# Kernel optimization log

Hardware: AMD Instinct MI355X
Metric: run time of the kernel (lower is better)

The kernel has to match this reference:

```python
import jax, jax.numpy as jnp
import numpy as np

FIELD_DIMS = [100000, 1000, 100, 50]
NUM_FEATURES = 12
NUM_CAT = len(FIELD_DIMS)
NUM_CONT = NUM_FEATURES - NUM_CAT
D = 32            # embed_dim
HID = [64, 32]
B, T = 1024, 200
BN_EPS = 1e-5


def setup_inputs() -> dict:
    key = jax.random.key(0)
    ks = jax.random.split(key, 32)
    # x: [B, T, F]; first NUM_CAT cols are integer category ids stored as float
    cat_cols = [jax.random.randint(ks[i], (B, T, 1), 0, FIELD_DIMS[i]).astype(jnp.float32)
                for i in range(NUM_CAT)]
    cont_cols = jax.random.normal(ks[4], (B, T, NUM_CONT), dtype=jnp.float32)
    x = jnp.concatenate(cat_cols + [cont_cols], axis=-1)
    s = 0.05
    inp = {"x": x}
    for i, fd in enumerate(FIELD_DIMS):
        inp[f"emb{i}"] = jax.random.normal(ks[5 + i], (fd, D), dtype=jnp.float32) * s
        inp[f"lin{i}"] = jax.random.normal(ks[9 + i], (fd, D), dtype=jnp.float32) * s
    # Conv1d(1, D, 1) per continuous field == per-field affine map scalar -> D
    inp["cont_w"]  = jax.random.normal(ks[13], (NUM_CONT, D), dtype=jnp.float32) * s
    inp["cont_b"]  = jax.random.normal(ks[14], (NUM_CONT, D), dtype=jnp.float32) * s
    inp["clin_w"]  = jax.random.normal(ks[15], (NUM_CONT, D), dtype=jnp.float32) * s
    inp["clin_b"]  = jax.random.normal(ks[16], (NUM_CONT, D), dtype=jnp.float32) * s
    inp["fin_bias"] = jnp.zeros((D,), dtype=jnp.float32)
    # DNN tower: kernel_size-1 Conv1d == dense over channel dim
    dims = [NUM_FEATURES * D] + HID
    for li in range(len(HID)):
        fan_in = dims[li]
        inp[f"w{li+1}"] = jax.random.normal(ks[17 + 4 * li], (HID[li], fan_in), dtype=jnp.float32) / np.sqrt(fan_in)
        inp[f"b{li+1}"] = jnp.zeros((HID[li],), dtype=jnp.float32)
        inp[f"g{li+1}"] = jnp.ones((HID[li],), dtype=jnp.float32)
        inp[f"beta{li+1}"] = jnp.zeros((HID[li],), dtype=jnp.float32)
    inp["w_out"] = jax.random.normal(ks[30], (D, HID[-1]), dtype=jnp.float32) / np.sqrt(HID[-1])
    inp["b_out"] = jnp.zeros((D,), dtype=jnp.float32)
    return inp


def _batchnorm(h, g, b):
    # training-mode BN over (batch, time), biased variance (torch default)
    mu = h.mean(axis=(0, 1))
    var = h.var(axis=(0, 1))
    return g * (h - mu) * jax.lax.rsqrt(var + BN_EPS) + b


def reference(x, emb0, emb1, emb2, emb3, lin0, lin1, lin2, lin3,
              cont_w, cont_b, clin_w, clin_b, fin_bias,
              w1, b1, g1, beta1, w2, b2, g2, beta2, w_out, b_out):
    embs = [emb0, emb1, emb2, emb3]
    lins = [lin0, lin1, lin2, lin3]
    cat_idx = x[..., :NUM_CAT].astype(jnp.int32)          # [B,T,C]
    xc = x[..., NUM_CAT:]                                  # [B,T,Nc]

    # per-field embeddings -> [B,T,F,D]
    cat_emb = jnp.stack([embs[i][cat_idx[..., i]] for i in range(NUM_CAT)], axis=2)
    cont_emb = xc[..., None] * cont_w + cont_b             # [B,T,Nc,D]
    emb_all = jnp.concatenate([cat_emb, cont_emb], axis=2)  # [B,T,F,D]

    # FM pairwise interaction (sum-of-squares trick)
    s = emb_all.sum(axis=2)                                # [B,T,D]
    interaction = 0.5 * (s * s - (emb_all * emb_all).sum(axis=2))

    # linear terms
    lin_cat = sum(lins[i][cat_idx[..., i]] for i in range(NUM_CAT))      # [B,T,D]
    lin_cont = (xc[..., None] * clin_w + clin_b).sum(axis=2)             # [B,T,D]
    linear = lin_cat + lin_cont + fin_bias

    # DNN tower (k=1 convs == dense over F*D channels); dropout omitted (eval)
    h = emb_all.reshape(B, T, NUM_FEATURES * D)
    h = jax.nn.relu(_batchnorm(h @ w1.T + b1, g1, beta1))
    h = jax.nn.relu(_batchnorm(h @ w2.T + b2, g2, beta2))
    dnn = h @ w_out.T + b_out                              # [B,T,D]

    return linear + interaction + dnn                      # [B,T,D]
```

## Files before the change

kernel.cpp:

```cpp
#include <hip/hip_runtime.h>
#include <hip/hip_bf16.h>

typedef __hip_bfloat16 bf16;

#define ROWS 204800
#define N_INV (1.0f / 204800.0f)

__device__ float g_stats[256];
__device__ float g_E1_1[1000 * 64];
__device__ float g_E1_2[100 * 64];
__device__ float g_E1_3[50 * 64];
__device__ float g_U[8 * 64];
__device__ float g_Vb[64];
__device__ bf16  g_h1p[ROWS * 64];
__device__ bf16  g_h2p[ROWS * 32];

__device__ __forceinline__ int clampi(int v, int hi) {
    return v < 0 ? 0 : (v > hi ? hi : v);
}

__global__ __launch_bounds__(64) void precompute_kernel(
    const float* __restrict__ emb1, const float* __restrict__ emb2, const float* __restrict__ emb3,
    const float* __restrict__ cont_w, const float* __restrict__ cont_b,
    const float* __restrict__ w1, const float* __restrict__ b1)
{
    int b = blockIdx.x;
    int k = threadIdx.x;
    __shared__ float row[32];

    if (b < 1150) {
        const float* tab; float* out; int i, colOff;
        if (b < 1000)      { tab = emb1; out = g_E1_1; i = b;        colOff = 32; }
        else if (b < 1100) { tab = emb2; out = g_E1_2; i = b - 1000; colOff = 64; }
        else               { tab = emb3; out = g_E1_3; i = b - 1100; colOff = 96; }
        if (k < 32) row[k] = tab[i * 32 + k];
        __syncthreads();
        const float* wr = w1 + k * 384 + colOff;
        float acc = 0.f;
        #pragma unroll
        for (int d = 0; d < 32; ++d) acc = fmaf(row[d], wr[d], acc);
        out[i * 64 + k] = acc;
    } else {
        g_stats[k]       = 0.f;
        g_stats[k + 64]  = 0.f;
        g_stats[k + 128] = 0.f;
        g_stats[k + 192] = 0.f;

        float vb = b1[k];
        #pragma unroll
        for (int j = 0; j < 8; ++j) {
            const float* wr = w1 + k * 384 + (4 + j) * 32;
            float u = 0.f;
            #pragma unroll
            for (int d = 0; d < 32; ++d) {
                float w = wr[d];
                u  = fmaf(cont_w[j * 32 + d], w, u);
                vb = fmaf(cont_b[j * 32 + d], w, vb);
            }
            g_U[j * 64 + k] = u;
        }
        g_Vb[k] = vb;
    }
}

__global__ __launch_bounds__(256) void phase1_kernel(
    const float* __restrict__ x,
    const float* __restrict__ emb0, const float* __restrict__ lin0,
    const float* __restrict__ emb1, const float* __restrict__ lin1,
    const float* __restrict__ emb2, const float* __restrict__ lin2,
    const float* __restrict__ emb3, const float* __restrict__ lin3,
    const float* __restrict__ cont_w, const float* __restrict__ cont_b,
    const float* __restrict__ clin_w, const float* __restrict__ clin_b,
    const float* __restrict__ fin_bias, const float* __restrict__ w1,
    float* __restrict__ fm_out)
{
    __shared__ float lsum[64], lsq[64];

    int tid  = threadIdx.x;
    int lane = tid & 63;
    int wv   = tid >> 6;
    int d    = lane & 31;
    bool lo  = lane < 32;

    if (tid < 64) { lsum[tid] = 0.f; lsq[tid] = 0.f; }
    __syncthreads();

    float w1col[32];
    {
        const float4* wr = (const float4*)(w1 + lane * 384);
        #pragma unroll
        for (int q = 0; q < 8; ++q) {
            float4 v = wr[q];
            w1col[4*q+0] = v.x; w1col[4*q+1] = v.y;
            w1col[4*q+2] = v.z; w1col[4*q+3] = v.w;
        }
    }
    float uk[8];
    #pragma unroll
    for (int j = 0; j < 8; ++j) uk[j] = g_U[j * 64 + lane];
    float vbk = g_Vb[lane];

    float p1[8], p2[8], fb = 0.f;
    if (lo) {
        #pragma unroll
        for (int j = 0; j < 8; ++j) { p1[j] = cont_w[j * 32 + d]; p2[j] = cont_b[j * 32 + d]; }
    } else {
        #pragma unroll
        for (int j = 0; j < 8; ++j) { p1[j] = clin_w[j * 32 + d]; p2[j] = clin_b[j * 32 + d]; }
        fb = fin_bias[d];
    }

    int gw   = blockIdx.x * 4 + wv;
    int base = gw * 25;
    float ss = 0.f, qq = 0.f;

    float xv = (lane < 12) ? x[base * 12 + lane] : 0.f;

    for (int it = 0; it < 25; ++it) {
        int r = base + it;

        int i0 = clampi((int)__shfl(xv, 0), 99999);
        int i1 = clampi((int)__shfl(xv, 1), 999);
        int i2 = clampi((int)__shfl(xv, 2), 99);
        int i3 = clampi((int)__shfl(xv, 3), 49);
        float xc[8];
        #pragma unroll
        for (int j = 0; j < 8; ++j) xc[j] = __shfl(xv, 4 + j);

        float ga, gb, gc, gd;
        if (lo) {
            ga = emb0[i0 * 32 + d]; gb = emb1[i1 * 32 + d];
            gc = emb2[i2 * 32 + d]; gd = emb3[i3 * 32 + d];
        } else {
            ga = lin0[i0 * 32 + d]; gb = lin1[i1 * 32 + d];
            gc = lin2[i2 * 32 + d]; gd = lin3[i3 * 32 + d];
        }
        float t1 = g_E1_1[i1 * 64 + lane];
        float t2 = g_E1_2[i2 * 64 + lane];
        float t3 = g_E1_3[i3 * 64 + lane];
        float xvn = (it < 24 && lane < 12) ? x[(r + 1) * 12 + lane] : 0.f;

        float half_val;
        if (lo) {
            float s = (ga + gb) + (gc + gd);
            float q = fmaf(ga, ga, gb * gb) + fmaf(gc, gc, gd * gd);
            #pragma unroll
            for (int j = 0; j < 8; ++j) {
                float ce = fmaf(xc[j], p1[j], p2[j]);
                s += ce;
                q = fmaf(ce, ce, q);
            }
            half_val = 0.5f * (s * s - q);
        } else {
            float l = (ga + gb) + (gc + gd) + fb;
            #pragma unroll
            for (int j = 0; j < 8; ++j) l = fmaf(xc[j], p1[j], l + p2[j]);
            half_val = l;
        }
        float other = __shfl(half_val, lane | 32);
        if (lo) fm_out[r * 32 + d] = half_val + other;

        float h1 = ((vbk + t1) + (t2 + t3));
        #pragma unroll
        for (int j = 0; j < 8; ++j) h1 = fmaf(xc[j], uk[j], h1);

        float a0 = 0.f, a1 = 0.f, a2 = 0.f, a3 = 0.f;
        #pragma unroll
        for (int dd = 0; dd < 32; dd += 4) {
            a0 = fmaf(__shfl(ga, dd + 0), w1col[dd + 0], a0);
            a1 = fmaf(__shfl(ga, dd + 1), w1col[dd + 1], a1);
            a2 = fmaf(__shfl(ga, dd + 2), w1col[dd + 2], a2);
            a3 = fmaf(__shfl(ga, dd + 3), w1col[dd + 3], a3);
        }
        h1 += (a0 + a1) + (a2 + a3);

        g_h1p[r * 64 + lane] = __float2bfloat16(h1);
        ss += h1;
        qq = fmaf(h1, h1, qq);
        xv = xvn;
    }

    atomicAdd(&lsum[lane], ss);
    atomicAdd(&lsq[lane], qq);
    __syncthreads();
    if (tid < 64) {
        atomicAdd(&g_stats[tid], lsum[tid]);
        atomicAdd(&g_stats[64 + tid], lsq[tid]);
    }
}

__global__ __launch_bounds__(256) void phase2_kernel(
    const float* __restrict__ w2, const float* __restrict__ b2,
    const float* __restrict__ g1, const float* __restrict__ beta1)
{
    __shared__ float lsum[32], lsq[32];

    int tid  = threadIdx.x;
    int lane = tid & 63;
    int wv   = tid >> 6;
    int m    = lane & 31;
    int h    = lane >> 5;

    if (tid < 32) { lsum[tid] = 0.f; lsq[tid] = 0.f; }
    __syncthreads();

    float w2h[32];
    {
        const float4* wr = (const float4*)(w2 + m * 64 + 32 * h);
        #pragma unroll
        for (int q = 0; q < 8; ++q) {
            float4 v = wr[q];
            w2h[4*q+0] = v.x; w2h[4*q+1] = v.y;
            w2h[4*q+2] = v.z; w2h[4*q+3] = v.w;
        }
    }

    float S  = g_stats[lane], Q = g_stats[64 + lane];
    float mu = S * N_INV;
    float var = Q * N_INV - mu * mu;
    float a1 = g1[lane] * rsqrtf(var + 1e-5f);
    float c1 = beta1[lane] - a1 * mu;
    float b2m = b2[m];

    int gw   = blockIdx.x * 4 + wv;
    int base = gw * 25;
    float ss = 0.f, qq = 0.f;

    bf16 hv = g_h1p[base * 64 + lane];

    for (int it = 0; it < 25; ++it) {
        int r = base + it;
        float y1 = fmaxf(0.f, fmaf(a1, __bfloat162float(hv), c1));
        if (it < 24) hv = g_h1p[(r + 1) * 64 + lane];

        float a0 = 0.f, aa1 = 0.f, a2 = 0.f, a3 = 0.f;
        #pragma unroll
        for (int kk = 0; kk < 32; kk += 4) {
            a0  = fmaf(__shfl(y1, 32 * h + kk + 0), w2h[kk + 0], a0);
            aa1 = fmaf(__shfl(y1, 32 * h + kk + 1), w2h[kk + 1], aa1);
            a2  = fmaf(__shfl(y1, 32 * h + kk + 2), w2h[kk + 2], a2);
            a3  = fmaf(__shfl(y1, 32 * h + kk + 3), w2h[kk + 3], a3);
        }
        float part = (a0 + aa1) + (a2 + a3);
        float h2 = part + __shfl_xor(part, 32) + b2m;

        if (h == 0) g_h2p[r * 32 + m] = __float2bfloat16(h2);
        ss += h2;
        qq = fmaf(h2, h2, qq);
    }

    atomicAdd(&lsum[m], ss);
    atomicAdd(&lsq[m], qq);
    __syncthreads();
    if (tid < 32) {
        atomicAdd(&g_stats[128 + tid], 0.5f * lsum[tid]);
        atomicAdd(&g_stats[160 + tid], 0.5f * lsq[tid]);
    }
}

__global__ __launch_bounds__(256) void phase3_kernel(
    const float* __restrict__ w_out, const float* __restrict__ b_out,
    const float* __restrict__ g2, const float* __restrict__ beta2,
    float* __restrict__ out)
{
    int tid  = threadIdx.x;
    int lane = tid & 63;
    int wv   = tid >> 6;
    int m    = lane & 31;
    int h    = lane >> 5;

    float wo[32];
    {
        const float4* wr = (const float4*)(w_out + m * 32);
        #pragma unroll
        for (int q = 0; q < 8; ++q) {
            float4 v = wr[q];
            wo[4*q+0] = v.x; wo[4*q+1] = v.y;
            wo[4*q+2] = v.z; wo[4*q+3] = v.w;
        }
    }

    float S  = g_stats[128 + m], Q = g_stats[160 + m];
    float mu = S * N_INV;
    float var = Q * N_INV - mu * mu;
    float a2 = g2[m] * rsqrtf(var + 1e-5f);
    float c2 = beta2[m] - a2 * mu;
    float bo = b_out[m];

    int gw   = blockIdx.x * 4 + wv;
    int base = gw * 50 + h * 25;

    bf16  hv = g_h2p[base * 32 + m];
    float fv = out[base * 32 + m];

    for (int it = 0; it < 25; ++it) {
        int r = base + it;
        float y2 = fmaxf(0.f, fmaf(a2, __bfloat162float(hv), c2));
        float o  = fv + bo;
        if (it < 24) {
            hv = g_h2p[(r + 1) * 32 + m];
            fv = out[(r + 1) * 32 + m];
        }

        float a0 = 0.f, a1 = 0.f, aa2 = 0.f, a3 = 0.f;
        #pragma unroll
        for (int k = 0; k < 32; k += 4) {
            a0  = fmaf(__shfl(y2, 32 * h + k + 0), wo[k + 0], a0);
            a1  = fmaf(__shfl(y2, 32 * h + k + 1), wo[k + 1], a1);
            aa2 = fmaf(__shfl(y2, 32 * h + k + 2), wo[k + 2], aa2);
            a3  = fmaf(__shfl(y2, 32 * h + k + 3), wo[k + 3], a3);
        }
        out[r * 32 + m] = o + (a0 + a1) + (aa2 + a3);
    }
}

extern "C" void kernel_launch(void* const* d_in, const int* in_sizes, int n_in,
                              void* d_out, int out_size, void* d_ws, size_t ws_size,
                              hipStream_t stream) {
    (void)in_sizes; (void)n_in; (void)out_size; (void)d_ws; (void)ws_size;

    const float* x       = (const float*)d_in[0];
    const float* emb0    = (const float*)d_in[1];
    const float* lin0    = (const float*)d_in[2];
    const float* emb1    = (const float*)d_in[3];
    const float* lin1    = (const float*)d_in[4];
    const float* emb2    = (const float*)d_in[5];
    const float* lin2    = (const float*)d_in[6];
    const float* emb3    = (const float*)d_in[7];
    const float* lin3    = (const float*)d_in[8];
    const float* cont_w  = (const float*)d_in[9];
    const float* cont_b  = (const float*)d_in[10];
    const float* clin_w  = (const float*)d_in[11];
    const float* clin_b  = (const float*)d_in[12];
    const float* fin_bias= (const float*)d_in[13];
    const float* w1      = (const float*)d_in[14];
    const float* b1      = (const float*)d_in[15];
    const float* g1      = (const float*)d_in[16];
    const float* beta1   = (const float*)d_in[17];
    const float* w2      = (const float*)d_in[18];
    const float* b2      = (const float*)d_in[19];
    const float* g2      = (const float*)d_in[20];
    const float* beta2   = (const float*)d_in[21];
    const float* w_out   = (const float*)d_in[22];
    const float* b_out   = (const float*)d_in[23];

    float* outp = (float*)d_out;

    hipLaunchKernelGGL(precompute_kernel, dim3(1151), dim3(64), 0, stream,
                       emb1, emb2, emb3, cont_w, cont_b, w1, b1);

    hipLaunchKernelGGL(phase1_kernel, dim3(2048), dim3(256), 0, stream,
                       x, emb0, lin0, emb1, lin1, emb2, lin2, emb3, lin3,
                       cont_w, cont_b, clin_w, clin_b, fin_bias, w1,
                       outp);

    hipLaunchKernelGGL(phase2_kernel, dim3(2048), dim3(256), 0, stream,
                       w2, b2, g1, beta1);

    hipLaunchKernelGGL(phase3_kernel, dim3(1024), dim3(256), 0, stream,
                       w_out, b_out, g2, beta2, outp);
}
```

Before: 394.8 us.

## Restructure phases to row-per-thread matmuls with batched gathers and separate BN prep

Result: slower. 505.5 us (+28.0%).

```diff
diff --git a/kernel.cpp b/kernel.cpp
--- a/kernel.cpp
+++ b/kernel.cpp
@@ -12,11 +12,16 @@
 __device__ float g_E1_3[50 * 64];
 __device__ float g_U[8 * 64];
 __device__ float g_Vb[64];
+__device__ float g_bn1[128];
+__device__ float g_bn2[64];
 __device__ bf16  g_h1p[ROWS * 64];
 __device__ bf16  g_h2p[ROWS * 32];
 
 __device__ __forceinline__ int clampi(int v, int hi) {
     return v < 0 ? 0 : (v > hi ? hi : v);
+}
+__device__ __forceinline__ float rl_f(float v, int l) {
+    return __uint_as_float((unsigned int)__builtin_amdgcn_readlane((int)__float_as_uint(v), l));
 }
 
 __global__ __launch_bounds__(64) void precompute_kernel(
@@ -110,40 +115,57 @@
         fb = fin_bias[d];
     }
 
+    const float* T0 = lo ? emb0 : lin0;
+    const float* T1 = lo ? emb1 : lin1;
+    const float* T2 = lo ? emb2 : lin2;
+    const float* T3 = lo ? emb3 : lin3;
+
     int gw   = blockIdx.x * 4 + wv;
-    int base = gw * 25;
+    int base = gw * 8;
+
+    float xa = (lane < 48) ? x[base * 12 + lane] : 0.f;
+    float xb = (lane < 48) ? x[base * 12 + 48 + lane] : 0.f;
+
+    int i0[8], i1[8], i2[8], i3[8];
+    #pragma unroll
+    for (int it = 0; it < 8; ++it) {
+        float s  = (it < 4) ? xa : xb;
+        int   f  = (it < 4) ? it * 12 : it * 12 - 48;
+        i0[it] = clampi((int)rl_f(s, f + 0), 99999);
+        i1[it] = clampi((int)rl_f(s, f + 1), 999);
+        i2[it] = clampi((int)rl_f(s, f + 2), 99);
+        i3[it] = clampi((int)rl_f(s, f + 3), 49);
+    }
+
+    float ga[8], gb[8], gc[8], gd[8], t1[8], t2[8], t3[8];
+    #pragma unroll
+    for (int it = 0; it < 8; ++it) {
+        ga[it] = T0[i0[it] * 32 + d];
+        gb[it] = T1[i1[it] * 32 + d];
+        gc[it] = T2[i2[it] * 32 + d];
+        gd[it] = T3[i3[it] * 32 + d];
+        t1[it] = g_E1_1[i1[it] * 64 + lane];
+        t2[it] = g_E1_2[i2[it] * 64 + lane];
+        t3[it] = g_E1_3[i3[it] * 64 + lane];
+    }
+
     float ss = 0.f, qq = 0.f;
 
-    float xv = (lane < 12) ? x[base * 12 + lane] : 0.f;
-
-    for (int it = 0; it < 25; ++it) {
+    #pragma unroll
+    for (int it = 0; it < 8; ++it) {
         int r = base + it;
-
-        int i0 = clampi((int)__shfl(xv, 0), 99999);
-        int i1 = clampi((int)__shfl(xv, 1), 999);
-        int i2 = clampi((int)__shfl(xv, 2), 99);
-        int i3 = clampi((int)__shfl(xv, 3), 49);
+        float xs = (it < 4) ? xa : xb;
+        int   fo = ((it < 4) ? it * 12 : it * 12 - 48) + 4;
         float xc[8];
         #pragma unroll
-        for (int j = 0; j < 8; ++j) xc[j] = __shfl(xv, 4 + j);
-
-        float ga, gb, gc, gd;
-        if (lo) {
-            ga = emb0[i0 * 32 + d]; gb = emb1[i1 * 32 + d];
-            gc = emb2[i2 * 32 + d]; gd = emb3[i3 * 32 + d];
-        } else {
-            ga = lin0[i0 * 32 + d]; gb = lin1[i1 * 32 + d];
-            gc = lin2[i2 * 32 + d]; gd = lin3[i3 * 32 + d];
-        }
-        float t1 = g_E1_1[i1 * 64 + lane];
-        float t2 = g_E1_2[i2 * 64 + lane];
-        float t3 = g_E1_3[i3 * 64 + lane];
-        float xvn = (it < 24 && lane < 12) ? x[(r + 1) * 12 + lane] : 0.f;
+        for (int j = 0; j < 8; ++j) xc[j] = rl_f(xs, fo + j);
+
+        float cga = ga[it], cgb = gb[it], cgc = gc[it], cgd = gd[it];
 
         float half_val;
         if (lo) {
-            float s = (ga + gb) + (gc + gd);
-            float q = fmaf(ga, ga, gb * gb) + fmaf(gc, gc, gd * gd);
+            float s = (cga + cgb) + (cgc + cgd);
+            float q = fmaf(cga, cga, cgb * cgb) + fmaf(cgc, cgc, cgd * cgd);
             #pragma unroll
             for (int j = 0; j < 8; ++j) {
                 float ce = fmaf(xc[j], p1[j], p2[j]);
@@ -152,7 +174,7 @@
             }
             half_val = 0.5f * (s * s - q);
         } else {
-            float l = (ga + gb) + (gc + gd) + fb;
+            float l = (cga + cgb) + (cgc + cgd) + fb;
             #pragma unroll
             for (int j = 0; j < 8; ++j) l = fmaf(xc[j], p1[j], l + p2[j]);
             half_val = l;
@@ -160,24 +182,22 @@
         float other = __shfl(half_val, lane | 32);
         if (lo) fm_out[r * 32 + d] = half_val + other;
 
-        float h1 = ((vbk + t1) + (t2 + t3));
+        float h1 = (vbk + t1[it]) + (t2[it] + t3[it]);
         #pragma unroll
         for (int j = 0; j < 8; ++j) h1 = fmaf(xc[j], uk[j], h1);
-
         float a0 = 0.f, a1 = 0.f, a2 = 0.f, a3 = 0.f;
         #pragma unroll
         for (int dd = 0; dd < 32; dd += 4) {
-            a0 = fmaf(__shfl(ga, dd + 0), w1col[dd + 0], a0);
-            a1 = fmaf(__shfl(ga, dd + 1), w1col[dd + 1], a1);
-            a2 = fmaf(__shfl(ga, dd + 2), w1col[dd + 2], a2);
-            a3 = fmaf(__shfl(ga, dd + 3), w1col[dd + 3], a3);
+            a0 = fmaf(rl_f(cga, dd + 0), w1col[dd + 0], a0);
+            a1 = fmaf(rl_f(cga, dd + 1), w1col[dd + 1], a1);
+            a2 = fmaf(rl_f(cga, dd + 2), w1col[dd + 2], a2);
+            a3 = fmaf(rl_f(cga, dd + 3), w1col[dd + 3], a3);
         }
         h1 += (a0 + a1) + (a2 + a3);
 
         g_h1p[r * 64 + lane] = __float2bfloat16(h1);
         ss += h1;
         qq = fmaf(h1, h1, qq);
-        xv = xvn;
     }
 
     atomicAdd(&lsum[lane], ss);
@@ -189,129 +209,167 @@
     }
 }
 
-__global__ __launch_bounds__(256) void phase2_kernel(
-    const float* __restrict__ w2, const float* __restrict__ b2,
+__global__ __launch_bounds__(64) void bnprep1_kernel(
     const float* __restrict__ g1, const float* __restrict__ beta1)
 {
-    __shared__ float lsum[32], lsq[32];
-
+    int k = threadIdx.x;
+    float mu  = g_stats[k] * N_INV;
+    float var = g_stats[64 + k] * N_INV - mu * mu;
+    float a   = g1[k] * rsqrtf(var + 1e-5f);
+    g_bn1[k]      = a;
+    g_bn1[64 + k] = beta1[k] - a * mu;
+}
+
+__global__ __launch_bounds__(256, 4) void phase2_kernel(
+    const float* __restrict__ w2, const float* __restrict__ b2)
+{
     int tid  = threadIdx.x;
     int lane = tid & 63;
     int wv   = tid >> 6;
-    int m    = lane & 31;
-    int h    = lane >> 5;
-
-    if (tid < 32) { lsum[tid] = 0.f; lsq[tid] = 0.f; }
+    int row  = (blockIdx.x * 4 + wv) * 64 + lane;
+
+    const uint4* hrow = (const uint4*)(g_h1p + (size_t)row * 64);
+    uint4 u[8];
+    #pragma unroll
+    for (int q = 0; q < 8; ++q) u[q] = hrow[q];
+
+    float y[64];
+    #pragma unroll
+    for (int q = 0; q < 8; ++q) {
+        unsigned int w4[4] = {u[q].x, u[q].y, u[q].z, u[q].w};
+        #pragma unroll
+        for (int j = 0; j < 4; ++j) {
+            int i = q * 4 + j;
+            float f0 = __uint_as_float(w4[j] << 16);
+            float f1 = __uint_as_float(w4[j] & 0xffff0000u);
+            y[2*i]     = fmaxf(0.f, g_bn1[2*i]     * f0 + g_bn1[64 + 2*i]);
+            y[2*i + 1] = fmaxf(0.f, g_bn1[2*i + 1] * f1 + g_bn1[64 + 2*i + 1]);
+        }
+    }
+
+    float h2v[32];
+    #pragma unroll
+    for (int m = 0; m < 32; ++m) {
+        const float* wr = w2 + m * 64;
+        float a0 = b2[m], a1 = 0.f, a2 = 0.f, a3 = 0.f;
+        #pragma unroll
+        for (int k = 0; k < 64; k += 4) {
+            a0 = fmaf(y[k + 0], wr[k + 0], a0);
+            a1 = fmaf(y[k + 1], wr[k + 1], a1);
+            a2 = fmaf(y[k + 2], wr[k + 2], a2);
+            a3 = fmaf(y[k + 3], wr[k + 3], a3);
+        }
+        h2v[m] = (a0 + a1) + (a2 + a3);
+    }
+
+    uint4 o[4];
+    unsigned int* ow = (unsigned int*)o;
+    #pragma unroll
+    for (int i = 0; i < 16; ++i) {
+        unsigned int lo16 = (unsigned int)__bfloat16_as_ushort(__float2bfloat16(h2v[2*i]));
+        unsigned int hi16 = (unsigned int)__bfloat16_as_ushort(__float2bfloat16(h2v[2*i + 1]));
+        ow[i] = lo16 | (hi16 << 16);
+    }
+    uint4* orow = (uint4*)(g_h2p + (size_t)row * 32);
+    #pragma unroll
+    for (int q = 0; q < 4; ++q) orow[q] = o[q];
+}
+
+__global__ __launch_bounds__(256) void red2_kernel()
+{
+    __shared__ float ls[64];
+    int tid = threadIdx.x;
+    if (tid < 64) ls[tid] = 0.f;
     __syncthreads();
 
-    float w2h[32];
-    {
-        const float4* wr = (const float4*)(w2 + m * 64 + 32 * h);
-        #pragma unroll
-        for (int q = 0; q < 8; ++q) {
-            float4 v = wr[q];
-            w2h[4*q+0] = v.x; w2h[4*q+1] = v.y;
-            w2h[4*q+2] = v.z; w2h[4*q+3] = v.w;
-        }
-    }
-
-    float S  = g_stats[lane], Q = g_stats[64 + lane];
-    float mu = S * N_INV;
-    float var = Q * N_INV - mu * mu;
-    float a1 = g1[lane] * rsqrtf(var + 1e-5f);
-    float c1 = beta1[lane] - a1 * mu;
-    float b2m = b2[m];
-
-    int gw   = blockIdx.x * 4 + wv;
-    int base = gw * 25;
-    float ss = 0.f, qq = 0.f;
-
-    bf16 hv = g_h1p[base * 64 + lane];
-
-    for (int it = 0; it < 25; ++it) {
-        int r = base + it;
-        float y1 = fmaxf(0.f, fmaf(a1, __bfloat162float(hv), c1));
-        if (it < 24) hv = g_h1p[(r + 1) * 64 + lane];
-
-        float a0 = 0.f, aa1 = 0.f, a2 = 0.f, a3 = 0.f;
-        #pragma unroll
-        for (int kk = 0; kk < 32; kk += 4) {
-            a0  = fmaf(__shfl(y1, 32 * h + kk + 0), w2h[kk + 0], a0);
-            aa1 = fmaf(__shfl(y1, 32 * h + kk + 1), w2h[kk + 1], aa1);
-            a2  = fmaf(__shfl(y1, 32 * h + kk + 2), w2h[kk + 2], a2);
-            a3  = fmaf(__shfl(y1, 32 * h + kk + 3), w2h[kk + 3], a3);
-        }
-        float part = (a0 + aa1) + (a2 + a3);
-        float h2 = part + __shfl_xor(part, 32) + b2m;
-
-        if (h == 0) g_h2p[r * 32 + m] = __float2bfloat16(h2);
-        ss += h2;
-        qq = fmaf(h2, h2, qq);
-    }
-
-    atomicAdd(&lsum[m], ss);
-    atomicAdd(&lsq[m], qq);
+    const unsigned int* p = (const unsigned int*)g_h2p;
+    int cp = tid & 15;
+    float s0 = 0.f, q0 = 0.f, s1 = 0.f, q1 = 0.f;
+    for (int i = blockIdx.x * 256 + tid; i < ROWS * 16; i += 256 * 256) {
+        unsigned int u = p[i];
+        float f0 = __uint_as_float(u << 16);
+        float f1 = __uint_as_float(u & 0xffff0000u);
+        s0 += f0; q0 = fmaf(f0, f0, q0);
+        s1 += f1; q1 = fmaf(f1, f1, q1);
+    }
+    atomicAdd(&ls[2*cp],      s0);
+    atomicAdd(&ls[2*cp + 1],  s1);
+    atomicAdd(&ls[32 + 2*cp], q0);
+    atomicAdd(&ls[33 + 2*cp], q1);
     __syncthreads();
-    if (tid < 32) {
-        atomicAdd(&g_stats[128 + tid], 0.5f * lsum[tid]);
-        atomicAdd(&g_stats[160 + tid], 0.5f * lsq[tid]);
-    }
-}
-
-__global__ __launch_bounds__(256) void phase3_kernel(
+    if (tid < 32)            atomicAdd(&g_stats[128 + tid], ls[tid]);
+    else if (tid < 64)       atomicAdd(&g_stats[160 + (tid - 32)], ls[tid]);
+}
+
+__global__ __launch_bounds__(32) void bnprep2_kernel(
+    const float* __restrict__ g2, const float* __restrict__ beta2)
+{
+    int m = threadIdx.x;
+    float mu  = g_stats[128 + m] * N_INV;
+    float var = g_stats[160 + m] * N_INV - mu * mu;
+    float a   = g2[m] * rsqrtf(var + 1e-5f);
+    g_bn2[m]      = a;
+    g_bn2[32 + m] = beta2[m] - a * mu;
+}
+
+__global__ __launch_bounds__(256, 4) void phase3_kernel(
     const float* __restrict__ w_out, const float* __restrict__ b_out,
-    const float* __restrict__ g2, const float* __restrict__ beta2,
     float* __restrict__ out)
 {
     int tid  = threadIdx.x;
     int lane = tid & 63;
     int wv   = tid >> 6;
-    int m    = lane & 31;
-    int h    = lane >> 5;
-
-    float wo[32];
+    int row  = (blockIdx.x * 4 + wv) * 64 + lane;
+
+    const uint4* hrow = (const uint4*)(g_h2p + (size_t)row * 32);
+    uint4 u[4];
+    #pragma unroll
+    for (int q = 0; q < 4; ++q) u[q] = hrow[q];
+
+    float fmv[32];
     {
-        const float4* wr = (const float4*)(w_out + m * 32);
+        const float4* frow = (const float4*)(out + (size_t)row * 32);
         #pragma unroll
         for (int q = 0; q < 8; ++q) {
-            float4 v = wr[q];
-            wo[4*q+0] = v.x; wo[4*q+1] = v.y;
-            wo[4*q+2] = v.z; wo[4*q+3] = v.w;
-        }
-    }
-
-    float S  = g_stats[128 + m], Q = g_stats[160 + m];
-    float mu = S * N_INV;
-    float var = Q * N_INV - mu * mu;
-    float a2 = g2[m] * rsqrtf(var + 1e-5f);
-    float c2 = beta2[m] - a2 * mu;
-    float bo = b_out[m];
-
-    int gw   = blockIdx.x * 4 + wv;
-    int base = gw * 50 + h * 25;
-
-    bf16  hv = g_h2p[base * 32 + m];
-    float fv = out[base * 32 + m];
-
-    for (int it = 0; it < 25; ++it) {
-        int r = base + it;
-        float y2 = fmaxf(0.f, fmaf(a2, __bfloat162float(hv), c2));
-        float o  = fv + bo;
-        if (it < 24) {
-            hv = g_h2p[(r + 1) * 32 + m];
-            fv = out[(r + 1) * 32 + m];
-        }
-
-        float a0 = 0.f, a1 = 0.f, aa2 = 0.f, a3 = 0.f;
+            float4 v = frow[q];
+            fmv[4*q+0] = v.x; fmv[4*q+1] = v.y;
+            fmv[4*q+2] = v.z; fmv[4*q+3] = v.w;
+        }
+    }
+
+    float y2[32];
+    #pragma unroll
+    for (int q = 0; q < 4; ++q) {
+        unsigned int w4[4] = {u[q].x, u[q].y, u[q].z, u[q].w};
+        #pragma unroll
+        for (int j = 0; j < 4; ++j) {
+            int i = q * 4 + j;
+            float f0 = __uint_as_float(w4[j] << 16);
+            float f1 = __uint_as_float(w4[j] & 0xffff0000u);
+            y2[2*i]     = fmaxf(0.f, g_bn2[2*i]     * f0 + g_bn2[32 + 2*i]);
+            y2[2*i + 1] = fmaxf(0.f, g_bn2[2*i + 1] * f1 + g_bn2[32 + 2*i + 1]);
+        }
+    }
+
+    float res[32];
+    #pragma unroll
+    for (int dd = 0; dd < 32; ++dd) {
+        const float* wr = w_out + dd * 32;
+        float a0 = fmv[dd] + b_out[dd], a1 = 0.f, a2 = 0.f, a3 = 0.f;
         #pragma unroll
         for (int k = 0; k < 32; k += 4) {
-            a0  = fmaf(__shfl(y2, 32 * h + k + 0), wo[k + 0], a0);
-            a1  = fmaf(__shfl(y2, 32 * h + k + 1), wo[k + 1], a1);
-            aa2 = fmaf(__shfl(y2, 32 * h + k + 2), wo[k + 2], aa2);
-            a3  = fmaf(__shfl(y2, 32 * h + k + 3), wo[k + 3], a3);
-        }
-        out[r * 32 + m] = o + (a0 + a1) + (aa2 + a3);
-    }
+            a0 = fmaf(y2[k + 0], wr[k + 0], a0);
+            a1 = fmaf(y2[k + 1], wr[k + 1], a1);
+            a2 = fmaf(y2[k + 2], wr[k + 2], a2);
+            a3 = fmaf(y2[k + 3], wr[k + 3], a3);
+        }
+        res[dd] = (a0 + a1) + (a2 + a3);
+    }
+
+    float4* orow = (float4*)(out + (size_t)row * 32);
+    #pragma unroll
+    for (int q = 0; q < 8; ++q)
+        orow[q] = make_float4(res[4*q+0], res[4*q+1], res[4*q+2], res[4*q+3]);
 }
 
 extern "C" void kernel_launch(void* const* d_in, const int* in_sizes, int n_in,
@@ -349,14 +407,19 @@
     hipLaunchKernelGGL(precompute_kernel, dim3(1151), dim3(64), 0, stream,
                        emb1, emb2, emb3, cont_w, cont_b, w1, b1);
 
-    hipLaunchKernelGGL(phase1_kernel, dim3(2048), dim3(256), 0, stream,
+    hipLaunchKernelGGL(phase1_kernel, dim3(6400), dim3(256), 0, stream,
                        x, emb0, lin0, emb1, lin1, emb2, lin2, emb3, lin3,
                        cont_w, cont_b, clin_w, clin_b, fin_bias, w1,
                        outp);
 
-    hipLaunchKernelGGL(phase2_kernel, dim3(2048), dim3(256), 0, stream,
-                       w2, b2, g1, beta1);
-
-    hipLaunchKernelGGL(phase3_kernel, dim3(1024), dim3(256), 0, stream,
-                       w_out, b_out, g2, beta2, outp);
-}
+    hipLaunchKernelGGL(bnprep1_kernel, dim3(1), dim3(64), 0, stream, g1, beta1);
+
+    hipLaunchKernelGGL(phase2_kernel, dim3(800), dim3(256), 0, stream, w2, b2);
+
+    hipLaunchKernelGGL(red2_kernel, dim3(256), dim3(256), 0, stream);
+
+    hipLaunchKernelGGL(bnprep2_kernel, dim3(1), dim3(32), 0, stream, g2, beta2);
+
+    hipLaunchKernelGGL(phase3_kernel, dim3(800), dim3(256), 0, stream,
+                       w_out, b_out, outp);
+}
```
